# Kernel optimization log

Hardware: AMD Instinct MI355X
Metric: run time of the kernel (lower is better)

## Reference

```python
import jax, jax.numpy as jnp
import numpy as np

B, N, D, H = 4, 2048, 256, 4
DH = D // H
SS = DH ** -0.25  # sqrt(scale), applied to both qk0 and qk1
EPS = 1e-5


def _split_heads(t):
    # [B, N, D] -> [B, H, N, DH]
    b, n, _ = t.shape
    return t.reshape(b, n, H, DH).transpose(0, 2, 1, 3)


def _merge_heads(t):
    # [B, H, N, DH] -> [B, N, D]
    b, h, n, dh = t.shape
    return t.transpose(0, 2, 1, 3).reshape(b, n, h * dh)


def _layernorm(x, g, b):
    mu = jnp.mean(x, axis=-1, keepdims=True)
    var = jnp.mean(jnp.square(x - mu), axis=-1, keepdims=True)
    return (x - mu) * jax.lax.rsqrt(var + EPS) * g + b


def setup_inputs() -> dict:
    key = jax.random.key(0)
    ks = jax.random.split(key, 16)
    s = 0.02
    return {
        "x0": jax.random.normal(ks[0], (B, N, D), jnp.float32),
        "x1": jax.random.normal(ks[1], (B, N, D), jnp.float32),
        # weights stored as [in, out] (y = x @ W + b), matching torch Linear math
        "Wqk": jax.random.normal(ks[2], (D, D), jnp.float32) * s,
        "bqk": jnp.zeros((D,), jnp.float32),
        "Wv": jax.random.normal(ks[3], (D, D), jnp.float32) * s,
        "bv": jnp.zeros((D,), jnp.float32),
        "Wo": jax.random.normal(ks[4], (D, D), jnp.float32) * s,
        "bo": jnp.zeros((D,), jnp.float32),
        "W1": jax.random.normal(ks[5], (2 * D, 2 * D), jnp.float32) * s,
        "b1": jnp.zeros((2 * D,), jnp.float32),
        "ln_g": jnp.ones((2 * D,), jnp.float32),
        "ln_b": jnp.zeros((2 * D,), jnp.float32),
        "W2": jax.random.normal(ks[6], (2 * D, D), jnp.float32) * s,
        "b2": jnp.zeros((D,), jnp.float32),
    }


def reference(x0, x1, Wqk, bqk, Wv, bv, Wo, bo, W1, b1, ln_g, ln_b, W2, b2):
    qk0 = _split_heads(x0 @ Wqk + bqk) * SS  # [B,H,N,DH]
    qk1 = _split_heads(x1 @ Wqk + bqk) * SS
    v0 = _split_heads(x0 @ Wv + bv)
    v1 = _split_heads(x1 @ Wv + bv)

    # single shared similarity matrix, reused for both softmax directions
    sim = jnp.einsum("bhid,bhjd->bhij", qk0, qk1)  # [B,H,N0,N1]
    attn01 = jax.nn.softmax(sim, axis=-1)                      # rows over j
    attn10 = jax.nn.softmax(jnp.swapaxes(sim, -1, -2), axis=-1)  # rows over i

    m0 = jnp.einsum("bhij,bhjd->bhid", attn01, v1)  # [B,H,N0,DH]
    m1 = jnp.einsum("bhji,bhjd->bhid", jnp.swapaxes(attn10, -1, -2), v0)

    m0 = _merge_heads(m0) @ Wo + bo  # [B,N,D]
    m1 = _merge_heads(m1) @ Wo + bo

    def ffn(x, m):
        h = jnp.concatenate([x, m], axis=-1) @ W1 + b1
        h = jax.nn.gelu(_layernorm(h, ln_g, ln_b), approximate=False)
        return x + h @ W2 + b2

    return ffn(x0, m0), ffn(x1, m1)
```

## Files before the change

kernel.cpp:

```cpp
#include <hip/hip_runtime.h>
#include <hip/hip_bf16.h>
#include <math.h>

#define DEV static __device__ __forceinline__

typedef float f32x4 __attribute__((ext_vector_type(4)));
typedef short s16x8 __attribute__((ext_vector_type(8)));
typedef unsigned short u16;
typedef unsigned int u32;
typedef u32 u32x2 __attribute__((ext_vector_type(2)));
typedef u16 u16x4 __attribute__((ext_vector_type(4)));
typedef u16 u16x8 __attribute__((ext_vector_type(8)));

#define SSCALE 0.35355339059327379f
#define SS2 0.42466089345200966f

DEV f32x4 mfma16(s16x8 a, s16x8 b, f32x4 c) {
  return __builtin_amdgcn_mfma_f32_16x16x32_bf16(a, b, c, 0, 0, 0);
}

DEV float bf2f(u16 x) { u32 u = ((u32)x) << 16; float f; __builtin_memcpy(&f, &u, 4); return f; }
DEV u16 f2bf(float x) { __hip_bfloat16 b = __float2bfloat16(x); u16 r; __builtin_memcpy(&r, &b, 2); return r; }

DEV float fexp2(float x) {
#if __has_builtin(__builtin_amdgcn_exp2f)
  return __builtin_amdgcn_exp2f(x);
#else
  return exp2f(x);
#endif
}

DEV void gload_lds16(const void* g, void* l) {
  __builtin_amdgcn_global_load_lds((const __attribute__((address_space(1))) u32*)g,
                                   (__attribute__((address_space(3))) u32*)l, 16, 0, 0);
}

__global__ __launch_bounds__(256) void k_prep(
    const float* __restrict__ x0, const float* __restrict__ x1,
    const float* __restrict__ Wqk, const float* __restrict__ Wv,
    const float* __restrict__ Wo, const float* __restrict__ W1,
    const float* __restrict__ W2, const float* __restrict__ bo,
    const float* __restrict__ b1,
    u16* __restrict__ btqkv, u16* __restrict__ btF,
    u16* __restrict__ bt2, float* __restrict__ bc, u16* __restrict__ Xb)
{
  const int blk = blockIdx.x, tid = threadIdx.x;
  if (blk < 2048) {
    int idx = blk * 2048 + tid * 8;
    const float* src = (idx < 2097152) ? (x0 + idx) : (x1 + (idx - 2097152));
    f32x4 va = *(const f32x4*)src;
    f32x4 vb = *(const f32x4*)(src + 4);
    u16x8 o;
#pragma unroll
    for (int j = 0; j < 4; ++j) { o[j] = f2bf(va[j]); o[4 + j] = f2bf(vb[j]); }
    *(u16x8*)(Xb + idx) = o;
  } else if (blk < 2144) {
    __shared__ float T[64][65];
    int tb = blk - 2048;
    const float* src; u16* dst; int sld, dld, kr0, c0, drow0;
    if (tb < 16)      { src = Wqk; dst = btqkv; sld = 256; dld = 256; drow0 = 0;
                        kr0 = (tb >> 2) * 64; c0 = (tb & 3) * 64; }
    else if (tb < 32) { tb -= 16; src = Wv; dst = btqkv; sld = 256; dld = 256; drow0 = 256;
                        kr0 = (tb >> 2) * 64; c0 = (tb & 3) * 64; }
    else if (tb < 64) { tb -= 32; src = W1; dst = btF; sld = 512; dld = 512; drow0 = 0;
                        kr0 = (tb >> 3) * 64; c0 = (tb & 7) * 64; }
    else              { tb -= 64; src = W2; dst = bt2; sld = 256; dld = 512; drow0 = 0;
                        kr0 = (tb >> 2) * 64; c0 = (tb & 3) * 64; }
    int r = tid >> 2, cq = (tid & 3) * 16;
#pragma unroll
    for (int q = 0; q < 4; ++q) {
      f32x4 v = *(const f32x4*)(src + (size_t)(kr0 + r) * sld + c0 + cq + q * 4);
#pragma unroll
      for (int e = 0; e < 4; ++e) T[r][cq + q * 4 + e] = v[e];
    }
    __syncthreads();
    int c = tid >> 2, kq = (tid & 3) * 16;
#pragma unroll
    for (int q = 0; q < 2; ++q) {
      u16x8 o;
#pragma unroll
      for (int e = 0; e < 8; ++e) o[e] = f2bf(T[kq + q * 8 + e][c]);
      *(u16x8*)(dst + (size_t)(drow0 + c0 + c) * dld + kr0 + kq + q * 8) = o;
    }
  } else if (blk < 2656) {
    int wb = blk - 2144;
    int i = wb >> 1;
    int n = (wb & 1) * 256 + tid;
    float a0 = 0.f, a1 = 0.f, a2 = 0.f, a3 = 0.f;
    for (int j = 0; j < 256; j += 4) {
      a0 = fmaf(Wo[i * 256 + j],     W1[(size_t)(256 + j) * 512 + n], a0);
      a1 = fmaf(Wo[i * 256 + j + 1], W1[(size_t)(257 + j) * 512 + n], a1);
      a2 = fmaf(Wo[i * 256 + j + 2], W1[(size_t)(258 + j) * 512 + n], a2);
      a3 = fmaf(Wo[i * 256 + j + 3], W1[(size_t)(259 + j) * 512 + n], a3);
    }
    btF[(size_t)n * 512 + 256 + i] = f2bf((a0 + a1) + (a2 + a3));
  } else {
    int n = (blk - 2656) * 256 + tid;
    float acc = b1[n];
    for (int j = 0; j < 256; ++j)
      acc = fmaf(bo[j], W1[(size_t)(256 + j) * 512 + n], acc);
    bc[n] = acc;
  }
}

template <int KD, int K1, int EPI, int BN>
__global__ __launch_bounds__(256, 2) void k_gemm(
    const u16* __restrict__ A1, const u16* __restrict__ A2,
    const u16* __restrict__ Bt,
    const float* __restrict__ bias, const float* __restrict__ bias2,
    const float* __restrict__ res0, const float* __restrict__ res1,
    u16* __restrict__ outb, u16* __restrict__ outb2,
    float* __restrict__ outf, int Ncols)
{
  constexpr int MR = (BN == 128) ? 4 : 2;
  __shared__ char lds[16384 + 2 * BN * 64];
  char* ldsA = lds;
  char* ldsB = lds + 16384;
  const int tid = threadIdx.x;
  const int lane = tid & 63;
  const int w = tid >> 6;
  const int wm = (BN == 128) ? (w >> 1) : w;
  const int wn = (BN == 128) ? (w & 1) : 0;
  const int g = lane >> 4, li = lane & 15;
  const int m0 = blockIdx.x * 128, n0 = blockIdx.y * BN;

  auto stage = [&](int buf, int t) {
    const int k0 = t * 32;
#pragma unroll
    for (int it = 0; it < 2; ++it) {
      int chunk = it * 256 + w * 64 + lane;
      int row = chunk >> 2, c = chunk & 3;
      int kc = k0 + ((c ^ ((row >> 1) & 3)) << 3);
      const u16* src = (kc < K1) ? (A1 + (size_t)(m0 + row) * K1 + kc)
                                 : (A2 + (size_t)(m0 + row) * (KD - K1) + (kc - K1));
      gload_lds16(src, ldsA + buf * 8192 + (it * 256 + w * 64) * 16);
    }
#pragma unroll
    for (int it = 0; it < BN / 64; ++it) {
      int chunk = it * 256 + w * 64 + lane;
      int row = chunk >> 2, c = chunk & 3;
      int kc = k0 + ((c ^ ((row >> 1) & 3)) << 3);
      gload_lds16(Bt + (size_t)(n0 + row) * KD + kc,
                  ldsB + buf * (BN * 64) + (it * 256 + w * 64) * 16);
    }
  };

  f32x4 acc[MR][4] = {};

  stage(0, 0);
  __syncthreads();
  const int NT = KD / 32;
  for (int t = 0; t < NT; ++t) {
    if (t + 1 < NT) stage((t + 1) & 1, t + 1);
    const char* bufA = ldsA + (t & 1) * 8192;
    const char* bufB = ldsB + (t & 1) * (BN * 64);
    s16x8 af[MR], bfr[4];
#pragma unroll
    for (int rt = 0; rt < MR; ++rt) {
      int row = wm * (MR * 16) + rt * 16 + li;
      af[rt] = *(const s16x8*)(bufA + row * 64 + ((g ^ ((row >> 1) & 3)) << 4));
    }
#pragma unroll
    for (int ct = 0; ct < 4; ++ct) {
      int col = wn * 64 + ct * 16 + li;
      bfr[ct] = *(const s16x8*)(bufB + col * 64 + ((g ^ ((col >> 1) & 3)) << 4));
    }
#pragma unroll
    for (int rt = 0; rt < MR; ++rt)
#pragma unroll
      for (int ct = 0; ct < 4; ++ct)
        acc[rt][ct] = mfma16(af[rt], bfr[ct], acc[rt][ct]);
    __syncthreads();
  }

#pragma unroll
  for (int rt = 0; rt < MR; ++rt) {
#pragma unroll
    for (int ct = 0; ct < 4; ++ct) {
      const int growb = m0 + wm * (MR * 16) + rt * 16 + g * 4;
      const int gcol = n0 + wn * 64 + ct * 16 + li;
      if (EPI == 0) {
        const int dir = growb >> 13, bb = (growb >> 11) & 3, n = growb & 2047;
        if (gcol < 256) {
          const int h = gcol >> 6, dh = gcol & 63;
#pragma unroll
          for (int r = 0; r < 4; ++r) {
            float q = (acc[rt][ct][r] + bias[gcol]) * SS2;
            outb[((size_t)(dir * 16 + bb * 4 + h) * 2048 + (n + r)) * 64 + dh] = f2bf(q);
          }
        } else {
          const int c2 = gcol - 256, h = c2 >> 6, dh = c2 & 63;
          u16x4 pk;
#pragma unroll
          for (int r = 0; r < 4; ++r) pk[r] = f2bf(acc[rt][ct][r] + bias2[c2]);
          *(u16x4*)(outb2 + ((size_t)(dir * 16 + bb * 4 + h) * 64 + dh) * 2048 + n) = pk;
        }
      } else if (EPI == 1) {
#pragma unroll
        for (int r = 0; r < 4; ++r)
          outb[(size_t)(growb + r) * Ncols + gcol] = f2bf(acc[rt][ct][r] + bias[gcol]);
      } else {
#pragma unroll
        for (int r = 0; r < 4; ++r) {
          int grow = growb + r;
          float x = (grow < 8192) ? res0[(size_t)grow * 256 + gcol]
                                  : res1[(size_t)(grow - 8192) * 256 + gcol];
          outf[(size_t)grow * 256 + gcol] = acc[rt][ct][r] + bias[gcol] + x;
        }
      }
    }
  }
}

__global__ __launch_bounds__(512, 4) void k_attn(
    const u16* __restrict__ qk, const u16* __restrict__ vt, u16* __restrict__ m_all)
{
  __shared__ char Kl[2][2][8192];
  __shared__ char Vl[2][2][8192];
  const int tid = threadIdx.x, lane = tid & 63, w = tid >> 6;
  const int half = w >> 2, wq = w & 3;
  const int g = lane >> 4, li = lane & 15;
  const int sw = (blockIdx.x & 7) * 64 + (blockIdx.x >> 3);
  const int qblk = sw & 15;
  const int p = sw >> 4;
  const int dir = p >> 4, bh = p & 15;
  const char* Qg = (const char*)qk + (size_t)p * 262144;
  const char* Kg = (const char*)qk + (size_t)((dir ^ 1) * 16 + bh) * 262144;
  const char* Vg = (const char*)vt + (size_t)((dir ^ 1) * 16 + bh) * 262144;
  const int q0 = qblk * 128 + wq * 32;
  const int perm = (li & 3) | ((li & 4) << 1) | ((li & 8) >> 1);

  s16x8 qf[2][2];
#pragma unroll
  for (int qt = 0; qt < 2; ++qt)
#pragma unroll
    for (int h = 0; h < 2; ++h)
      qf[qt][h] = *(const s16x8*)(Qg + (size_t)(q0 + qt * 16 + li) * 128 + h * 64 + g * 16);

  auto stageKV = [&](int buf, int jt) {
    const int kb = half * 1024 + jt * 64;
#pragma unroll
    for (int it = 0; it < 2; ++it) {
      int chunk = it * 256 + wq * 64 + lane;
      int row = chunk >> 3, c = chunk & 7;
      int cc = (c ^ (row & 7)) << 4;
      gload_lds16(Kg + (size_t)(kb + row) * 128 + cc, &Kl[half][buf][chunk * 16]);
    }
#pragma unroll
    for (int it = 0; it < 2; ++it) {
      int chunk = it * 256 + wq * 64 + lane;
      int row = chunk >> 3, c = chunk & 7;
      int cc = (c ^ (row & 7)) << 4;
      gload_lds16(Vg + (size_t)row * 4096 + kb * 2 + cc, &Vl[half][buf][chunk * 16]);
    }
  };

  f32x4 acco[2][4] = {};
  float accl[2] = {0.f, 0.f};

  stageKV(0, 0);
  __syncthreads();
  for (int jt = 0; jt < 16; ++jt) {
    if (jt + 1 < 16) stageKV((jt + 1) & 1, jt + 1);
    const char* Kb = &Kl[half][jt & 1][0];
    const char* Vb = &Vl[half][jt & 1][0];

    u32 pw[4][2][2];
#pragma unroll
    for (int kt = 0; kt < 4; ++kt) {
      const int krow = kt * 16 + perm;
      s16x8 kf0 = *(const s16x8*)(Kb + krow * 128 + ((g ^ (krow & 7)) << 4));
      s16x8 kf1 = *(const s16x8*)(Kb + krow * 128 + (((4 + g) ^ (krow & 7)) << 4));
#pragma unroll
      for (int qt = 0; qt < 2; ++qt) {
        f32x4 s = {0.f, 0.f, 0.f, 0.f};
        s = mfma16(kf0, qf[qt][0], s);
        s = mfma16(kf1, qf[qt][1], s);
        float p0 = fexp2(s[0]), p1 = fexp2(s[1]);
        float p2 = fexp2(s[2]), p3 = fexp2(s[3]);
        accl[qt] += (p0 + p1) + (p2 + p3);
        pw[kt][qt][0] = (u32)f2bf(p0) | ((u32)f2bf(p1) << 16);
        pw[kt][qt][1] = (u32)f2bf(p2) | ((u32)f2bf(p3) << 16);
      }
    }

    s16x8 pf[2][2];
#pragma unroll
    for (int ks = 0; ks < 2; ++ks)
#pragma unroll
      for (int qt = 0; qt < 2; ++qt) {
        u32 a0 = pw[ks * 2][qt][0], b0 = pw[ks * 2 + 1][qt][0];
        u32 a1 = pw[ks * 2][qt][1], b1 = pw[ks * 2 + 1][qt][1];
        asm("v_permlane32_swap_b32 %0, %1" : "+v"(a0), "+v"(b0));
        asm("v_permlane32_swap_b32 %0, %1" : "+v"(a1), "+v"(b1));
        u32 words[4] = {a0, a1, b0, b1};
        __builtin_memcpy(&pf[ks][qt], words, 16);
      }

#pragma unroll
    for (int ks = 0; ks < 2; ++ks)
#pragma unroll
      for (int dt = 0; dt < 4; ++dt) {
        const int vrow = dt * 16 + li;
        s16x8 vfr = *(const s16x8*)(Vb + vrow * 128 + (((ks * 4 + g) ^ (vrow & 7)) << 4));
        acco[0][dt] = mfma16(pf[ks][0], vfr, acco[0][dt]);
        acco[1][dt] = mfma16(pf[ks][1], vfr, acco[1][dt]);
      }
    __syncthreads();
  }

#pragma unroll
  for (int qt = 0; qt < 2; ++qt) {
    float v = accl[qt];
    v += __shfl_xor(v, 16);
    v += __shfl_xor(v, 32);
    accl[qt] = v;
  }

  float* scr  = (float*)&Kl[0][0][0];
  float* lscr = (float*)&Vl[0][0][0];
  if (half == 0) {
#pragma unroll
    for (int qt = 0; qt < 2; ++qt)
#pragma unroll
      for (int dt = 0; dt < 4; ++dt)
        *(f32x4*)(scr + wq * 2048 + lane * 32 + (((qt * 4 + dt) * 4) ^ ((lane & 7) << 2))) =
            acco[qt][dt];
    if (lane < 16) {
      lscr[wq * 32 + li] = accl[0];
      lscr[wq * 32 + 16 + li] = accl[1];
    }
  }
  __syncthreads();
  if (half == 1) {
    float invq[2][4];
#pragma unroll
    for (int qt = 0; qt < 2; ++qt) {
      float ltot = accl[qt] + lscr[wq * 32 + qt * 16 + li];
      float inv = 1.0f / ltot;
#pragma unroll
      for (int r = 0; r < 4; ++r) invq[qt][r] = __shfl(inv, g * 4 + r);
    }
    const int bb = bh >> 2, h = bh & 3;
#pragma unroll
    for (int qt = 0; qt < 2; ++qt) {
      const size_t rowb = (size_t)dir * 8192 + (size_t)bb * 2048 + q0 + qt * 16 + g * 4;
#pragma unroll
      for (int dt = 0; dt < 4; ++dt) {
        f32x4 o = *(const f32x4*)(scr + wq * 2048 + lane * 32 +
                                  (((qt * 4 + dt) * 4) ^ ((lane & 7) << 2)));
#pragma unroll
        for (int r = 0; r < 4; ++r)
          m_all[(rowb + r) * 256 + h * 64 + dt * 16 + li] =
              f2bf((acco[qt][dt][r] + o[r]) * invq[qt][r]);
      }
    }
  }
}

__global__ __launch_bounds__(256) void k_ln_gelu(
    const u16* __restrict__ h, const float* __restrict__ lg,
    const float* __restrict__ lb, u16* __restrict__ o)
{
  int lane = threadIdx.x & 63;
  size_t row = blockIdx.x * 4 + (threadIdx.x >> 6);
  s16x8 v = *(const s16x8*)(h + row * 512 + lane * 8);
  float f[8], s = 0.f, s2 = 0.f;
#pragma unroll
  for (int j = 0; j < 8; ++j) { f[j] = bf2f((u16)v[j]); s += f[j]; s2 += f[j] * f[j]; }
#pragma unroll
  for (int m = 1; m < 64; m <<= 1) { s += __shfl_xor(s, m); s2 += __shfl_xor(s2, m); }
  float mu = s * (1.0f / 512.0f);
  float var = s2 * (1.0f / 512.0f) - mu * mu;
  float rs = rsqrtf(var + 1e-5f);
  s16x8 ov;
#pragma unroll
  for (int j = 0; j < 8; ++j) {
    int c = lane * 8 + j;
    float y = (f[j] - mu) * rs * lg[c] + lb[c];
    float ge = 0.5f * y * (1.0f + erff(y * 0.70710678118654752f));
    ov[j] = (short)f2bf(ge);
  }
  *(s16x8*)(o + row * 512 + lane * 8) = ov;
}

extern "C" void kernel_launch(void* const* d_in, const int* in_sizes, int n_in,
                              void* d_out, int out_size, void* d_ws, size_t ws_size,
                              hipStream_t stream)
{
  const float* x0  = (const float*)d_in[0];
  const float* x1  = (const float*)d_in[1];
  const float* Wqk = (const float*)d_in[2];
  const float* bqk = (const float*)d_in[3];
  const float* Wv  = (const float*)d_in[4];
  const float* bv  = (const float*)d_in[5];
  const float* Wo  = (const float*)d_in[6];
  const float* bo  = (const float*)d_in[7];
  const float* W1  = (const float*)d_in[8];
  const float* b1  = (const float*)d_in[9];
  const float* lg  = (const float*)d_in[10];
  const float* lb  = (const float*)d_in[11];
  const float* W2  = (const float*)d_in[12];
  const float* b2  = (const float*)d_in[13];
  float* out = (float*)d_out;
  char* ws = (char*)d_ws;

  u16*   Xb    = (u16*)(ws + 0);
  u16*   qk    = (u16*)(ws + 8388608);
  u16*   vt    = (u16*)(ws + 16777216);
  u16*   m_all = (u16*)(ws + 25165824);
  u16*   hpre  = (u16*)(ws + 33554432);
  u16*   gact  = (u16*)(ws + 50331648);
  u16*   btqkv = (u16*)(ws + 67108864);
  u16*   btF   = (u16*)(ws + 67371008);
  u16*   bt2   = (u16*)(ws + 67895296);
  float* bc    = (float*)(ws + 68419584);

  k_prep<<<dim3(2658), dim3(256), 0, stream>>>(x0, x1, Wqk, Wv, Wo, W1, W2, bo, b1,
                                               btqkv, btF, bt2, bc, Xb);
  k_gemm<256, 256, 0, 128><<<dim3(128, 4), dim3(256), 0, stream>>>(
      Xb, nullptr, btqkv, bqk, bv, nullptr, nullptr, qk, vt, nullptr, 512);
  k_attn<<<dim3(512), dim3(512), 0, stream>>>(qk, vt, m_all);
  k_gemm<512, 256, 1, 128><<<dim3(128, 4), dim3(256), 0, stream>>>(
      Xb, m_all, btF, bc, nullptr, nullptr, nullptr, hpre, nullptr, nullptr, 512);
  k_ln_gelu<<<dim3(4096), dim3(256), 0, stream>>>(hpre, lg, lb, gact);
  k_gemm<512, 512, 3, 64><<<dim3(128, 4), dim3(256), 0, stream>>>(
      gact, nullptr, bt2, b2, nullptr, x0, x1, nullptr, nullptr, out, 256);
}
```

Baseline: 223.4 us.

## Read V directly from global, compute softmax row sums via MFMA ones

The attention kernel no longer stages V tiles into LDS; each wave reads V fragments straight from global memory (relying on cache), which halves LDS use and the async copy traffic. Softmax denominators are now accumulated with an extra MFMA against a ones vector, using the bf16-rounded probabilities, instead of scalar adds and cross-lane shuffles. Exp outputs are packed with a single v_cvt_pk_bf16_f32 instruction, and the prep kernel's weight-folding loops get 8-way accumulator unrolling. The cost is global load latency sitting directly in the inner loop plus extra MFMA work, and the denominators now come from rounded values.

```diff
diff --git a/kernel.cpp b/kernel.cpp
--- a/kernel.cpp
+++ b/kernel.cpp
@@ -8,7 +8,6 @@
 typedef short s16x8 __attribute__((ext_vector_type(8)));
 typedef unsigned short u16;
 typedef unsigned int u32;
-typedef u32 u32x2 __attribute__((ext_vector_type(2)));
 typedef u16 u16x4 __attribute__((ext_vector_type(4)));
 typedef u16 u16x8 __attribute__((ext_vector_type(8)));
 
@@ -21,6 +20,12 @@
 
 DEV float bf2f(u16 x) { u32 u = ((u32)x) << 16; float f; __builtin_memcpy(&f, &u, 4); return f; }
 DEV u16 f2bf(float x) { __hip_bfloat16 b = __float2bfloat16(x); u16 r; __builtin_memcpy(&r, &b, 2); return r; }
+
+DEV u32 cvtpk(float lo, float hi) {
+  u32 r;
+  asm("v_cvt_pk_bf16_f32 %0, %1, %2" : "=v"(r) : "v"(lo), "v"(hi));
+  return r;
+}
 
 DEV float fexp2(float x) {
 #if __has_builtin(__builtin_amdgcn_exp2f)
@@ -86,20 +91,23 @@
     int wb = blk - 2144;
     int i = wb >> 1;
     int n = (wb & 1) * 256 + tid;
-    float a0 = 0.f, a1 = 0.f, a2 = 0.f, a3 = 0.f;
-    for (int j = 0; j < 256; j += 4) {
-      a0 = fmaf(Wo[i * 256 + j],     W1[(size_t)(256 + j) * 512 + n], a0);
-      a1 = fmaf(Wo[i * 256 + j + 1], W1[(size_t)(257 + j) * 512 + n], a1);
-      a2 = fmaf(Wo[i * 256 + j + 2], W1[(size_t)(258 + j) * 512 + n], a2);
-      a3 = fmaf(Wo[i * 256 + j + 3], W1[(size_t)(259 + j) * 512 + n], a3);
-    }
-    btF[(size_t)n * 512 + 256 + i] = f2bf((a0 + a1) + (a2 + a3));
+    float a[8] = {0.f, 0.f, 0.f, 0.f, 0.f, 0.f, 0.f, 0.f};
+    for (int j = 0; j < 256; j += 8) {
+#pragma unroll
+      for (int e = 0; e < 8; ++e)
+        a[e] = fmaf(Wo[i * 256 + j + e], W1[(size_t)(256 + j + e) * 512 + n], a[e]);
+    }
+    btF[(size_t)n * 512 + 256 + i] =
+        f2bf(((a[0] + a[1]) + (a[2] + a[3])) + ((a[4] + a[5]) + (a[6] + a[7])));
   } else {
     int n = (blk - 2656) * 256 + tid;
-    float acc = b1[n];
-    for (int j = 0; j < 256; ++j)
-      acc = fmaf(bo[j], W1[(size_t)(256 + j) * 512 + n], acc);
-    bc[n] = acc;
+    float p[8] = {0.f, 0.f, 0.f, 0.f, 0.f, 0.f, 0.f, 0.f};
+    for (int j = 0; j < 256; j += 8) {
+#pragma unroll
+      for (int e = 0; e < 8; ++e)
+        p[e] = fmaf(bo[j + e], W1[(size_t)(256 + j + e) * 512 + n], p[e]);
+    }
+    bc[n] = b1[n] + (((p[0] + p[1]) + (p[2] + p[3])) + ((p[4] + p[5]) + (p[6] + p[7])));
   }
 }
 
@@ -216,7 +224,7 @@
     const u16* __restrict__ qk, const u16* __restrict__ vt, u16* __restrict__ m_all)
 {
   __shared__ char Kl[2][2][8192];
-  __shared__ char Vl[2][2][8192];
+  __shared__ float lsmall[128];
   const int tid = threadIdx.x, lane = tid & 63, w = tid >> 6;
   const int half = w >> 2, wq = w & 3;
   const int g = lane >> 4, li = lane & 15;
@@ -226,7 +234,7 @@
   const int dir = p >> 4, bh = p & 15;
   const char* Qg = (const char*)qk + (size_t)p * 262144;
   const char* Kg = (const char*)qk + (size_t)((dir ^ 1) * 16 + bh) * 262144;
-  const char* Vg = (const char*)vt + (size_t)((dir ^ 1) * 16 + bh) * 262144;
+  const u16*  Vg = vt + (size_t)((dir ^ 1) * 16 + bh) * 131072;
   const int q0 = qblk * 128 + wq * 32;
   const int perm = (li & 3) | ((li & 4) << 1) | ((li & 8) >> 1);
 
@@ -237,7 +245,11 @@
     for (int h = 0; h < 2; ++h)
       qf[qt][h] = *(const s16x8*)(Qg + (size_t)(q0 + qt * 16 + li) * 128 + h * 64 + g * 16);
 
-  auto stageKV = [&](int buf, int jt) {
+  s16x8 onesf;
+#pragma unroll
+  for (int e = 0; e < 8; ++e) onesf[e] = (short)0x3F80;
+
+  auto stageK = [&](int buf, int jt) {
     const int kb = half * 1024 + jt * 64;
 #pragma unroll
     for (int it = 0; it < 2; ++it) {
@@ -246,24 +258,17 @@
       int cc = (c ^ (row & 7)) << 4;
       gload_lds16(Kg + (size_t)(kb + row) * 128 + cc, &Kl[half][buf][chunk * 16]);
     }
-#pragma unroll
-    for (int it = 0; it < 2; ++it) {
-      int chunk = it * 256 + wq * 64 + lane;
-      int row = chunk >> 3, c = chunk & 7;
-      int cc = (c ^ (row & 7)) << 4;
-      gload_lds16(Vg + (size_t)row * 4096 + kb * 2 + cc, &Vl[half][buf][chunk * 16]);
-    }
   };
 
   f32x4 acco[2][4] = {};
-  float accl[2] = {0.f, 0.f};
-
-  stageKV(0, 0);
+  f32x4 accs[2] = {};
+
+  stageK(0, 0);
   __syncthreads();
   for (int jt = 0; jt < 16; ++jt) {
-    if (jt + 1 < 16) stageKV((jt + 1) & 1, jt + 1);
+    if (jt + 1 < 16) stageK((jt + 1) & 1, jt + 1);
     const char* Kb = &Kl[half][jt & 1][0];
-    const char* Vb = &Vl[half][jt & 1][0];
+    const int keyb = half * 1024 + jt * 64;
 
     u32 pw[4][2][2];
 #pragma unroll
@@ -276,11 +281,8 @@
         f32x4 s = {0.f, 0.f, 0.f, 0.f};
         s = mfma16(kf0, qf[qt][0], s);
         s = mfma16(kf1, qf[qt][1], s);
-        float p0 = fexp2(s[0]), p1 = fexp2(s[1]);
-        float p2 = fexp2(s[2]), p3 = fexp2(s[3]);
-        accl[qt] += (p0 + p1) + (p2 + p3);
-        pw[kt][qt][0] = (u32)f2bf(p0) | ((u32)f2bf(p1) << 16);
-        pw[kt][qt][1] = (u32)f2bf(p2) | ((u32)f2bf(p3) << 16);
+        pw[kt][qt][0] = cvtpk(fexp2(s[0]), fexp2(s[1]));
+        pw[kt][qt][1] = cvtpk(fexp2(s[2]), fexp2(s[3]));
       }
     }
 
@@ -298,27 +300,21 @@
       }
 
 #pragma unroll
-    for (int ks = 0; ks < 2; ++ks)
+    for (int ks = 0; ks < 2; ++ks) {
+      accs[0] = mfma16(pf[ks][0], onesf, accs[0]);
+      accs[1] = mfma16(pf[ks][1], onesf, accs[1]);
 #pragma unroll
       for (int dt = 0; dt < 4; ++dt) {
-        const int vrow = dt * 16 + li;
-        s16x8 vfr = *(const s16x8*)(Vb + vrow * 128 + (((ks * 4 + g) ^ (vrow & 7)) << 4));
+        s16x8 vfr = *(const s16x8*)(Vg + (size_t)(dt * 16 + li) * 2048 +
+                                    keyb + ks * 32 + g * 8);
         acco[0][dt] = mfma16(pf[ks][0], vfr, acco[0][dt]);
         acco[1][dt] = mfma16(pf[ks][1], vfr, acco[1][dt]);
       }
+    }
     __syncthreads();
   }
 
-#pragma unroll
-  for (int qt = 0; qt < 2; ++qt) {
-    float v = accl[qt];
-    v += __shfl_xor(v, 16);
-    v += __shfl_xor(v, 32);
-    accl[qt] = v;
-  }
-
-  float* scr  = (float*)&Kl[0][0][0];
-  float* lscr = (float*)&Vl[0][0][0];
+  float* scr = (float*)&Kl[0][0][0];
   if (half == 0) {
 #pragma unroll
     for (int qt = 0; qt < 2; ++qt)
@@ -326,24 +322,23 @@
       for (int dt = 0; dt < 4; ++dt)
         *(f32x4*)(scr + wq * 2048 + lane * 32 + (((qt * 4 + dt) * 4) ^ ((lane & 7) << 2))) =
             acco[qt][dt];
-    if (lane < 16) {
-      lscr[wq * 32 + li] = accl[0];
-      lscr[wq * 32 + 16 + li] = accl[1];
+    if (li == 0) {
+#pragma unroll
+      for (int qt = 0; qt < 2; ++qt)
+#pragma unroll
+        for (int r = 0; r < 4; ++r)
+          lsmall[wq * 32 + qt * 16 + g * 4 + r] = accs[qt][r];
     }
   }
   __syncthreads();
   if (half == 1) {
-    float invq[2][4];
+    const int bb = bh >> 2, h = bh & 3;
 #pragma unroll
     for (int qt = 0; qt < 2; ++qt) {
-      float ltot = accl[qt] + lscr[wq * 32 + qt * 16 + li];
-      float inv = 1.0f / ltot;
-#pragma unroll
-      for (int r = 0; r < 4; ++r) invq[qt][r] = __shfl(inv, g * 4 + r);
-    }
-    const int bb = bh >> 2, h = bh & 3;
-#pragma unroll
-    for (int qt = 0; qt < 2; ++qt) {
+      f32x4 lo = *(const f32x4*)(lsmall + wq * 32 + qt * 16 + g * 4);
+      f32x4 inv;
+#pragma unroll
+      for (int r = 0; r < 4; ++r) inv[r] = 1.0f / (accs[qt][r] + lo[r]);
       const size_t rowb = (size_t)dir * 8192 + (size_t)bb * 2048 + q0 + qt * 16 + g * 4;
 #pragma unroll
       for (int dt = 0; dt < 4; ++dt) {
@@ -352,7 +347,7 @@
 #pragma unroll
         for (int r = 0; r < 4; ++r)
           m_all[(rowb + r) * 256 + h * 64 + dt * 16 + li] =
-              f2bf((acco[qt][dt][r] + o[r]) * invq[qt][r]);
+              f2bf((acco[qt][dt][r] + o[r]) * inv[r]);
       }
     }
   }
```

New measurement: 251.5 us. 12.6% more time.
